# Performance work log

Hardware: AMD Instinct MI355X
Metric: run time of the kernel (lower is better)

Reference implementation:

```python
import jax, jax.numpy as jnp
from jax import lax
import numpy as np

B, S, V, H, C = 128, 512, 128, 1024, 10
E = H // 4  # embed_dim = hidden_dim / 4 per the module


def setup_inputs() -> dict:
    key = jax.random.key(0)
    ks = jax.random.split(key, 16)

    def kaiming(k, shape):
        fan_in = shape[0]
        return jax.random.normal(k, shape, dtype=jnp.float32) * np.sqrt(2.0 / fan_in)

    return {
        "x": jax.random.randint(ks[0], (B, 1, S), 0, V),
        "embedding": jax.random.normal(ks[1], (V, E), dtype=jnp.float32),
        "W_gx": kaiming(ks[2], (E, H)), "W_gh": kaiming(ks[3], (H, H)), "b_g": jnp.zeros((H,), jnp.float32),
        "W_ix": kaiming(ks[4], (E, H)), "W_ih": kaiming(ks[5], (H, H)), "b_i": jnp.zeros((H,), jnp.float32),
        "W_fx": kaiming(ks[6], (E, H)), "W_fh": kaiming(ks[7], (H, H)), "b_f": jnp.zeros((H,), jnp.float32),
        "W_ox": kaiming(ks[8], (E, H)), "W_oh": kaiming(ks[9], (H, H)), "b_o": jnp.zeros((H,), jnp.float32),
        "W_ph": kaiming(ks[10], (H, C)), "b_p": jnp.zeros((C,), jnp.float32),
    }


def reference(x, embedding, W_gx, W_gh, b_g, W_ix, W_ih, b_i,
              W_fx, W_fh, b_f, W_ox, W_oh, b_o, W_ph, b_p):
    batch = x.shape[0]
    hid = W_gh.shape[0]
    # embed whole sequence at once: [B, S, E]
    xe = embedding[x[:, 0, :]]
    # fuse the 4 input-side GEMMs into one: [B, S, 4H] (precomputable, parallel over time)
    Wx = jnp.concatenate([W_gx, W_ix, W_fx, W_ox], axis=1)  # [E, 4H]
    Wh = jnp.concatenate([W_gh, W_ih, W_fh, W_oh], axis=1)  # [H, 4H]
    b = jnp.concatenate([b_g, b_i, b_f, b_o])               # [4H]
    xproj = jnp.einsum('bse,ef->sbf', xe, Wx) + b           # [S, B, 4H] (time-major for scan)

    def step(carry, xp_t):
        h, c = carry
        z = xp_t + h @ Wh  # [B, 4H]
        g = jnp.tanh(z[:, :hid])
        i = jax.nn.sigmoid(z[:, hid:2 * hid])
        f = jax.nn.sigmoid(z[:, 2 * hid:3 * hid])
        o = jax.nn.sigmoid(z[:, 3 * hid:])
        c = g * i + c * f
        h = jnp.tanh(c) * o
        return (h, c), None

    h0 = jnp.zeros((batch, hid), xproj.dtype)
    c0 = jnp.zeros((batch, hid), xproj.dtype)
    (h, _), _ = lax.scan(step, (h0, c0), xproj)

    p = h @ W_ph + b_p
    return jax.nn.log_softmax(p, axis=1)
```

## Files before the change

kernel.cpp:

```cpp
#include <hip/hip_runtime.h>

#define H_ 1024
#define B_ 128
#define S_ 512
#define V_ 128
#define E_ 256

#define ZSH_OFF 0
#define TSH_OFF 67584
#define XSH_OFF 135168
#define SMEM_TOTAL 135232

#define HXBUF 131072

typedef __bf16 bf16x8 __attribute__((ext_vector_type(8)));
typedef float f32x4 __attribute__((ext_vector_type(4)));
typedef unsigned long long ull;

__device__ __forceinline__ uint4 cload16(const unsigned short* p) {
  uint4 r;
  asm volatile("global_load_dwordx4 %0, %1, off sc0 sc1"
               : "=v"(r) : "v"(p) : "memory");
  return r;
}
__device__ __forceinline__ void cstore8(unsigned short* p, ull v) {
  __hip_atomic_store((ull*)p, v, __ATOMIC_RELAXED, __HIP_MEMORY_SCOPE_AGENT);
}

__device__ __forceinline__ unsigned short f2bf(float f) {
  unsigned u = __float_as_uint(f);
  u += 0x7fffu + ((u >> 16) & 1u);
  return (unsigned short)(u >> 16);
}
__device__ __forceinline__ float sigf(float x) { return 1.0f / (1.0f + __expf(-x)); }
__device__ __forceinline__ float tanhfast(float x) { return 1.0f - 2.0f / (1.0f + __expf(2.0f * x)); }

__global__ void __launch_bounds__(256)
prep_kernel(const float* __restrict__ emb,
            const float* __restrict__ Wgx, const float* __restrict__ Wix,
            const float* __restrict__ Wfx, const float* __restrict__ Wox,
            const float* __restrict__ bg, const float* __restrict__ bi,
            const float* __restrict__ bf_, const float* __restrict__ bo,
            const float* __restrict__ Wgh, const float* __restrict__ Wih,
            const float* __restrict__ Wfh, const float* __restrict__ Woh,
            const int* __restrict__ x,
            float* __restrict__ tokproj, unsigned short* __restrict__ WhT,
            int* __restrict__ xT) {
  __shared__ float esh[E_];
  const int bid = blockIdx.x;
  if (bid < 2048) {
    const int v = bid >> 4;
    const int c = (bid & 15) * 256 + threadIdx.x;
    const int gate = c >> 10;
    const int j = c & 1023;
    const float* W = (gate == 0) ? Wgx : (gate == 1) ? Wix : (gate == 2) ? Wfx : Wox;
    const float* bias = (gate == 0) ? bg : (gate == 1) ? bi : (gate == 2) ? bf_ : bo;
    esh[threadIdx.x] = emb[v * E_ + threadIdx.x];
    __syncthreads();
    float acc = bias[j];
#pragma unroll 4
    for (int e = 0; e < E_; ++e) acc += esh[e] * W[e * H_ + j];
    tokproj[v * 4096 + c] = acc;
  } else if (bid < 6144) {
    const int c = bid - 2048;
    const int gate = c >> 10;
    const int j = c & 1023;
    const float* W = (gate == 0) ? Wgh : (gate == 1) ? Wih : (gate == 2) ? Wfh : Woh;
    for (int k = threadIdx.x; k < H_; k += 256)
      WhT[c * H_ + k] = f2bf(W[k * H_ + j]);
  } else {
    const int id = (bid - 6144) * 256 + threadIdx.x;
    const int s = id >> 7, b = id & 127;
    xT[s * 128 + b] = x[b * S_ + s];
  }
}

__global__ void __launch_bounds__(512, 1)
lstm_scan(const int* __restrict__ xT, const float* __restrict__ tokproj,
          const unsigned short* __restrict__ WhT,
          unsigned short* __restrict__ hX, float* __restrict__ hfin,
          unsigned* __restrict__ pub) {
  extern __shared__ char smem[];
  float* Zsh = (float*)(smem + ZSH_OFF);
  float* tsh = (float*)(smem + TSH_OFF);
  int* xsh = (int*)(smem + XSH_OFF);

  const int bid = blockIdx.x;
  const int rg = bid >> 5;
  const int cg = bid & 31;
  const int tid = threadIdx.x;
  const int w = tid >> 6;
  const int lane = tid & 63;
  const int l15 = lane & 15;
  const int lq = lane >> 4;

  for (int it = tid; it < 16384; it += 512) {
    const int v = it >> 7, j = it & 127;
    const int gate = j >> 5, hu = j & 31;
    tsh[(v * 33 + hu) * 4 + gate] = tokproj[v * 4096 + gate * 1024 + cg * 32 + hu];
  }
  uint4 breg[32];
#pragma unroll
  for (int kc = 0; kc < 4; ++kc) {
#pragma unroll
    for (int t = 0; t < 8; ++t) {
      const int j = t * 16 + l15;
      const int c = ((j >> 5) << 10) + cg * 32 + (j & 31);
      breg[kc * 8 + t] =
          *(const uint4*)(WhT + c * 1024 + (w * 4 + kc) * 32 + lq * 8);
    }
  }

  const int row_own = tid >> 5;
  const int hu = tid & 31;
  const int brow = rg * 16 + row_own;
  const int colg = cg * 32 + hu;

  const unsigned* myflag = pub + (rg * 32 + w * 4 + (lane & 3)) * 32;
  const unsigned short* abase[4];
#pragma unroll
  for (int kc = 0; kc < 4; ++kc)
    abase[kc] = hX + (rg * 32 + w * 4 + kc) * 512 + lane * 8;

  float creg = 0.f;
  if (tid < 128) cstore8(hX + bid * 512 + tid * 4, 0ull);
  asm volatile("s_waitcnt vmcnt(0)" ::: "memory");
  __syncthreads();
  if (tid == 0)
    __hip_atomic_store(pub + bid * 32, 1u, __ATOMIC_RELAXED, __HIP_MEMORY_SCOPE_AGENT);

  for (int s = 0; s < S_; ++s) {
    int xv = 0;
    if (tid < 16) xv = xT[s * 128 + rg * 16 + tid];

    const unsigned tgt = (unsigned)(s + 1);
    while (__hip_atomic_load(myflag, __ATOMIC_RELAXED, __HIP_MEMORY_SCOPE_AGENT) < tgt)
      __builtin_amdgcn_s_sleep(1);

    const int soff = (s & 1) * HXBUF;
    uint4 a[4];
#pragma unroll
    for (int kc = 0; kc < 4; ++kc) a[kc] = cload16(abase[kc] + soff);
    asm volatile("s_waitcnt vmcnt(0)" ::: "memory");
    __builtin_amdgcn_sched_barrier(0);
#pragma unroll
    for (int kc = 0; kc < 4; ++kc) {
      asm volatile("" : "+v"(a[kc].x), "+v"(a[kc].y), "+v"(a[kc].z), "+v"(a[kc].w));
    }

    if (tid < 16) xsh[tid] = xv;

    f32x4 acc[8];
#pragma unroll
    for (int t = 0; t < 8; ++t) acc[t] = (f32x4){0.f, 0.f, 0.f, 0.f};
#pragma unroll
    for (int kc = 0; kc < 4; ++kc) {
      const bf16x8 av = __builtin_bit_cast(bf16x8, a[kc]);
#pragma unroll
      for (int t = 0; t < 8; ++t)
        acc[t] = __builtin_amdgcn_mfma_f32_16x16x32_bf16(
            av, __builtin_bit_cast(bf16x8, breg[kc * 8 + t]), acc[t], 0, 0, 0);
    }
#pragma unroll
    for (int r_ = 0; r_ < 4; ++r_) {
      const int row = w * 16 + lq * 4 + r_;
      f32x4 lo = {acc[0][r_], acc[2][r_], acc[4][r_], acc[6][r_]};
      f32x4 hi = {acc[1][r_], acc[3][r_], acc[5][r_], acc[7][r_]};
      *(f32x4*)(Zsh + (row * 33 + l15) * 4) = lo;
      *(f32x4*)(Zsh + (row * 33 + l15 + 16) * 4) = hi;
    }
    __syncthreads();

    {
      const int xb = xsh[row_own];
      f32x4 z4 = *(const f32x4*)(tsh + (xb * 33 + hu) * 4);
#pragma unroll
      for (int w8 = 0; w8 < 8; ++w8)
        z4 += *(const f32x4*)(Zsh + ((w8 * 16 + row_own) * 33 + hu) * 4);
      const float gv = tanhfast(z4[0]);
      const float iv = sigf(z4[1]);
      const float fv = sigf(z4[2]);
      const float ov = sigf(z4[3]);
      creg = gv * iv + creg * fv;
      const float hv = tanhfast(creg) * ov;
      if (s == S_ - 1) hfin[brow * H_ + colg] = hv;

      const unsigned hvu = (unsigned)f2bf(hv);
      const unsigned o1 = (unsigned)__shfl_xor((int)hvu, 1);
      const unsigned p01 = (hvu & 0xFFFFu) | (o1 << 16);
      const unsigned o2 = (unsigned)__shfl_xor((int)p01, 2);
      const ull q = (ull)p01 | ((ull)o2 << 32);

      if ((lane & 3) == 0) {
        const int prow = 2 * w + (lane >> 5);
        const int hu0 = lane & 31;
        unsigned short* dst = hX + ((s + 1) & 1) * HXBUF + bid * 512
                              + (prow + ((hu0 >> 3) << 4)) * 8 + (hu0 & 7);
        cstore8(dst, q);
      }
    }
    asm volatile("s_waitcnt vmcnt(0)" ::: "memory");
    __syncthreads();
    if (tid == 0)
      __hip_atomic_store(pub + bid * 32, (unsigned)(s + 2),
                         __ATOMIC_RELAXED, __HIP_MEMORY_SCOPE_AGENT);
  }
}

__global__ void __launch_bounds__(256)
classify_kernel(const float* __restrict__ hfin, const float* __restrict__ Wph,
                const float* __restrict__ bp, float* __restrict__ out) {
  __shared__ float red[256 * 10];
  const int b = blockIdx.x, tid = threadIdx.x;
  float acc[10];
#pragma unroll
  for (int c = 0; c < 10; ++c) acc[c] = 0.f;
  for (int k = tid; k < H_; k += 256) {
    const float hv = hfin[b * H_ + k];
    const float* w = Wph + k * 10;
#pragma unroll
    for (int c = 0; c < 10; ++c) acc[c] += hv * w[c];
  }
#pragma unroll
  for (int c = 0; c < 10; ++c) red[tid * 10 + c] = acc[c];
  __syncthreads();
  for (int off = 128; off >= 1; off >>= 1) {
    if (tid < off) {
#pragma unroll
      for (int c = 0; c < 10; ++c) red[tid * 10 + c] += red[(tid + off) * 10 + c];
    }
    __syncthreads();
  }
  if (tid == 0) {
    float p[10];
    float m = -1e30f;
#pragma unroll
    for (int c = 0; c < 10; ++c) { p[c] = red[c] + bp[c]; m = fmaxf(m, p[c]); }
    float ssum = 0.f;
#pragma unroll
    for (int c = 0; c < 10; ++c) ssum += __expf(p[c] - m);
    const float lse = m + __logf(ssum);
#pragma unroll
    for (int c = 0; c < 10; ++c) out[b * 10 + c] = p[c] - lse;
  }
}

extern "C" void kernel_launch(void* const* d_in, const int* in_sizes, int n_in,
                              void* d_out, int out_size, void* d_ws, size_t ws_size,
                              hipStream_t stream) {
  (void)in_sizes; (void)n_in; (void)out_size; (void)ws_size;
  const int* x = (const int*)d_in[0];
  const float* emb = (const float*)d_in[1];
  const float* Wgx = (const float*)d_in[2];
  const float* Wgh = (const float*)d_in[3];
  const float* bg = (const float*)d_in[4];
  const float* Wix = (const float*)d_in[5];
  const float* Wih = (const float*)d_in[6];
  const float* bi = (const float*)d_in[7];
  const float* Wfx = (const float*)d_in[8];
  const float* Wfh = (const float*)d_in[9];
  const float* bf_ = (const float*)d_in[10];
  const float* Wox = (const float*)d_in[11];
  const float* Woh = (const float*)d_in[12];
  const float* bo = (const float*)d_in[13];
  const float* Wph = (const float*)d_in[14];
  const float* bp = (const float*)d_in[15];
  float* out = (float*)d_out;

  char* ws = (char*)d_ws;
  float* tokproj = (float*)ws;
  unsigned short* WhT = (unsigned short*)(ws + 2097152);
  unsigned short* hX = (unsigned short*)(ws + 10485760);
  float* hfin = (float*)(ws + 11010048);
  int* xT = (int*)(ws + 11538432);
  unsigned* pub = (unsigned*)(ws + 11800576);

  (void)hipMemsetAsync(pub, 0, 32768, stream);
  (void)hipFuncSetAttribute(reinterpret_cast<const void*>(lstm_scan),
                            hipFuncAttributeMaxDynamicSharedMemorySize, SMEM_TOTAL);

  prep_kernel<<<dim3(6400), dim3(256), 0, stream>>>(
      emb, Wgx, Wix, Wfx, Wox, bg, bi, bf_, bo,
      Wgh, Wih, Wfh, Woh, x, tokproj, WhT, xT);
  lstm_scan<<<dim3(256), dim3(512), SMEM_TOTAL, stream>>>(
      xT, tokproj, WhT, hX, hfin, pub);
  classify_kernel<<<dim3(128), dim3(256), 0, stream>>>(hfin, Wph, bp, out);
}
```

Before: 1.676 ms.

## Use NaN-sentinel triple-buffered h exchange to drop store-drain wait

Moves the hidden-state exchange buffer from double to triple buffering. The next-next buffer is poisoned with an all-ones sentinel, and readers spin on the loaded data until no sentinel remains. This removes the vmcnt(0) wait on stores before the flag publish, so flag and data visibility are no longer ordered. The cost is extra sentinel stores, possible re-polling loads, and a guarded loop that could read stale data if the guard expires.

Result: faster. 1.613 ms (-3.8%).

```diff
diff --git a/kernel.cpp b/kernel.cpp
--- a/kernel.cpp
+++ b/kernel.cpp
@@ -16,6 +16,9 @@
 typedef __bf16 bf16x8 __attribute__((ext_vector_type(8)));
 typedef float f32x4 __attribute__((ext_vector_type(4)));
 typedef unsigned long long ull;
+
+#define NANP 0xFFFFFFFFu
+#define NAN8 0xFFFFFFFFFFFFFFFFull
 
 __device__ __forceinline__ uint4 cload16(const unsigned short* p) {
   uint4 r;
@@ -122,6 +125,10 @@
   for (int kc = 0; kc < 4; ++kc)
     abase[kc] = hX + (rg * 32 + w * 4 + kc) * 512 + lane * 8;
 
+  const int prow = 2 * w + (lane >> 5);
+  const int hu0 = lane & 31;
+  const int choff = (prow + ((hu0 >> 3) << 4)) * 8 + (hu0 & 7);
+
   float creg = 0.f;
   if (tid < 128) cstore8(hX + bid * 512 + tid * 4, 0ull);
   asm volatile("s_waitcnt vmcnt(0)" ::: "memory");
@@ -129,6 +136,10 @@
   if (tid == 0)
     __hip_atomic_store(pub + bid * 32, 1u, __ATOMIC_RELAXED, __HIP_MEMORY_SCOPE_AGENT);
 
+  int bcur = 0;
+  int bnxt = 1;
+  int brst = 2;
+
   for (int s = 0; s < S_; ++s) {
     int xv = 0;
     if (tid < 16) xv = xT[s * 128 + rg * 16 + tid];
@@ -137,11 +148,26 @@
     while (__hip_atomic_load(myflag, __ATOMIC_RELAXED, __HIP_MEMORY_SCOPE_AGENT) < tgt)
       __builtin_amdgcn_s_sleep(1);
 
-    const int soff = (s & 1) * HXBUF;
+    const int soff = bcur * HXBUF;
     uint4 a[4];
-#pragma unroll
-    for (int kc = 0; kc < 4; ++kc) a[kc] = cload16(abase[kc] + soff);
-    asm volatile("s_waitcnt vmcnt(0)" ::: "memory");
+    {
+      int need0 = 1, need1 = 1, need2 = 1, need3 = 1;
+      int guard = 0;
+      for (;;) {
+        if (need0) a[0] = cload16(abase[0] + soff);
+        if (need1) a[1] = cload16(abase[1] + soff);
+        if (need2) a[2] = cload16(abase[2] + soff);
+        if (need3) a[3] = cload16(abase[3] + soff);
+        asm volatile("s_waitcnt vmcnt(0)" ::: "memory");
+        if (need0) need0 = !__all((int)((a[0].x != NANP) & (a[0].z != NANP)));
+        if (need1) need1 = !__all((int)((a[1].x != NANP) & (a[1].z != NANP)));
+        if (need2) need2 = !__all((int)((a[2].x != NANP) & (a[2].z != NANP)));
+        if (need3) need3 = !__all((int)((a[3].x != NANP) & (a[3].z != NANP)));
+        if (!(need0 | need1 | need2 | need3)) break;
+        if (++guard > (1 << 14)) break;
+        __builtin_amdgcn_s_sleep(1);
+      }
+    }
     __builtin_amdgcn_sched_barrier(0);
 #pragma unroll
     for (int kc = 0; kc < 4; ++kc) {
@@ -170,6 +196,9 @@
       *(f32x4*)(Zsh + (row * 33 + l15 + 16) * 4) = hi;
     }
     __syncthreads();
+
+    if ((lane & 3) == 0)
+      cstore8(hX + brst * HXBUF + bid * 512 + choff, NAN8);
 
     {
       const int xb = xsh[row_own];
@@ -191,19 +220,15 @@
       const unsigned o2 = (unsigned)__shfl_xor((int)p01, 2);
       const ull q = (ull)p01 | ((ull)o2 << 32);
 
-      if ((lane & 3) == 0) {
-        const int prow = 2 * w + (lane >> 5);
-        const int hu0 = lane & 31;
-        unsigned short* dst = hX + ((s + 1) & 1) * HXBUF + bid * 512
-                              + (prow + ((hu0 >> 3) << 4)) * 8 + (hu0 & 7);
-        cstore8(dst, q);
-      }
-    }
-    asm volatile("s_waitcnt vmcnt(0)" ::: "memory");
+      if ((lane & 3) == 0)
+        cstore8(hX + bnxt * HXBUF + bid * 512 + choff, q);
+    }
     __syncthreads();
     if (tid == 0)
       __hip_atomic_store(pub + bid * 32, (unsigned)(s + 2),
                          __ATOMIC_RELAXED, __HIP_MEMORY_SCOPE_AGENT);
+
+    const int t_ = bcur; bcur = bnxt; bnxt = brst; brst = t_;
   }
 }
 
@@ -271,10 +296,11 @@
   float* tokproj = (float*)ws;
   unsigned short* WhT = (unsigned short*)(ws + 2097152);
   unsigned short* hX = (unsigned short*)(ws + 10485760);
-  float* hfin = (float*)(ws + 11010048);
-  int* xT = (int*)(ws + 11538432);
-  unsigned* pub = (unsigned*)(ws + 11800576);
-
+  float* hfin = (float*)(ws + 11272192);
+  int* xT = (int*)(ws + 11796480);
+  unsigned* pub = (unsigned*)(ws + 12058624);
+
+  (void)hipMemsetAsync(hX, 0xFF, 786432, stream);
   (void)hipMemsetAsync(pub, 0, 32768, stream);
   (void)hipFuncSetAttribute(reinterpret_cast<const void*>(lstm_scan),
                             hipFuncAttributeMaxDynamicSharedMemorySize, SMEM_TOTAL);
```
